# Kernel tuning notes

Hardware: AMD Instinct MI355X
Metric: run time of the kernel (lower is better)

The kernel has to match this reference:

```python
import jax, jax.numpy as jnp
import numpy as np
import math

HID = 512
HEADS = 8
DK = HID // HEADS
B, S, T = 8, 4096, 512


def setup_inputs() -> dict:
    key = jax.random.key(0)
    ks = jax.random.split(key, 12)
    scale = 0.02
    inp = {
        "inputs": jax.random.normal(ks[0], (B, S, HID), dtype=jnp.float32),
        "targets": jax.random.normal(ks[1], (B, T, HID), dtype=jnp.float32),
        "mask": jnp.ones((B, S), dtype=bool),
        "Wq": jax.random.normal(ks[2], (HID, HID), dtype=jnp.float32) * scale,
        "bq": jnp.zeros((HID,), dtype=jnp.float32),
        "Wk": jax.random.normal(ks[3], (HID, HID), dtype=jnp.float32) * scale,
        "bk": jnp.zeros((HID,), dtype=jnp.float32),
        "Wv": jax.random.normal(ks[4], (HID, HID), dtype=jnp.float32) * scale,
        "bv": jnp.zeros((HID,), dtype=jnp.float32),
        "Wo": jax.random.normal(ks[5], (HID, HID), dtype=jnp.float32) * scale,
        "bo": jnp.zeros((HID,), dtype=jnp.float32),
    }
    return inp


def reference(inputs, targets, mask, Wq, bq, Wk, bk, Wv, bv, Wo, bo):
    # PoolingFunction(method='multihead-attention'), dropout=0 (identity),
    # hidden_size == output_size so mapping_function is identity.
    b, t, h = targets.shape
    s = inputs.shape[1]
    Q = (targets @ Wq.T + bq).reshape(b, t, HEADS, DK)
    K = (inputs @ Wk.T + bk).reshape(b, s, HEADS, DK)
    V = (inputs @ Wv.T + bv).reshape(b, s, HEADS, DK)
    # scores: b x heads x tgt x seq (same math as (Q*K).sum(-1)/sqrt(d_k))
    e = jnp.einsum('bthd,bshd->bhts', Q, K) / math.sqrt(DK)
    neg = (1.0 - mask.astype(jnp.float32)) * -1e20  # b x s
    e = e + neg[:, None, None, :]
    a = jax.nn.softmax(e, axis=-1)  # softmax over seq dim
    ctx = jnp.einsum('bhts,bshd->bthd', a, V).reshape(b, t, h)
    return ctx @ Wo.T + bo
```

## Files before the change

kernel.cpp:

```cpp
#include <hip/hip_runtime.h>
#include <hip/hip_bf16.h>
#include <cstdint>
#include <cstddef>

#define HIDN   512
#define NHEADS 8
#define BATCH  8
#define SLEN   4096
#define TLEN   512
#define SSPLIT 4
#define SCHUNK (SLEN / SSPLIT)
#define SCL2   0.18033688f

typedef __attribute__((ext_vector_type(8))) short   bf16x8;
typedef __attribute__((ext_vector_type(4))) float   f32x4;
typedef unsigned short u16;
typedef unsigned int   u32;

__device__ __forceinline__ u32 pkbf(float a, float b) {
    __hip_bfloat162 h = __float22bfloat162_rn(float2{a, b});
    union { __hip_bfloat162 h; u32 u; } un; un.h = h; return un.u;
}
__device__ __forceinline__ u32 pk2(float a, float b) {
    union { float f; u32 u; } ua, ub; ua.f = a; ub.f = b;
    return __builtin_amdgcn_perm(ub.u + 0x8000u, ua.u + 0x8000u, 0x07060302u);
}
__device__ __forceinline__ void gload_lds16(const u16* g, u16* l) {
    __builtin_amdgcn_global_load_lds(
        (const __attribute__((address_space(1))) u32*)g,
        (__attribute__((address_space(3))) u32*)l, 16, 0, 0);
}

__global__ __launch_bounds__(256) void cvt_all(
    const float* __restrict__ X, const float* __restrict__ Tg,
    const float* __restrict__ Wq, const float* __restrict__ Wk,
    const float* __restrict__ Wv, const float* __restrict__ Wo,
    const int* __restrict__ mask,
    u16* __restrict__ Xc, u16* __restrict__ Tc, u16* __restrict__ Wc,
    float* __restrict__ negf)
{
    int i4 = blockIdx.x * 256 + threadIdx.x;
    if (i4 >= 4980736) {
        int off = i4 - 4980736;
        int4 mv = ((const int4*)mask)[off];
        float4 nv;
        nv.x = mv.x ? 0.f : -1e30f; nv.y = mv.y ? 0.f : -1e30f;
        nv.z = mv.z ? 0.f : -1e30f; nv.w = mv.w ? 0.f : -1e30f;
        ((float4*)negf)[off] = nv;
        return;
    }
    const float* s; u16* d; long off;
    if (i4 < 4194304)      { s = X;  d = Xc; off = i4; }
    else if (i4 < 4718592) { s = Tg; d = Tc; off = i4 - 4194304; }
    else {
        int wi = i4 - 4718592; int widx = wi >> 16;
        s = (widx == 0) ? Wq : (widx == 1) ? Wk : (widx == 2) ? Wv : Wo;
        d = Wc + widx * 262144; off = wi & 65535;
    }
    float4 v = *(const float4*)(s + off * 4);
    uint2 o; o.x = pkbf(v.x, v.y); o.y = pkbf(v.z, v.w);
    *(uint2*)(d + off * 4) = o;
}

template<int MODE, int SEQ>
__global__ __launch_bounds__(256)
void gemm_bf16(const u16* __restrict__ A, const u16* __restrict__ Bw,
               const float* __restrict__ bias, void* __restrict__ Yv)
{
    __shared__ u16 As[128 * 32];
    __shared__ u16 Bs[128 * 32];
    const int tid = threadIdx.x;
    const int lane = tid & 63, w = tid >> 6;
    const int m = lane & 15, qd = lane >> 4;
    const int wm = w >> 1, wn = w & 1;
    const int m0 = blockIdx.y * 128, n0 = blockIdx.x * 128;

    f32x4 acc[4][4];
#pragma unroll
    for (int i = 0; i < 4; ++i)
#pragma unroll
        for (int j = 0; j < 4; ++j) acc[i][j] = (f32x4){0.f, 0.f, 0.f, 0.f};

    for (int k0 = 0; k0 < HIDN; k0 += 32) {
#pragma unroll
        for (int r = 0; r < 2; ++r) {
            const int f = tid + r * 256;
            const int row = f >> 2, c8 = (f & 3) * 8;
            const int fb = f & ~63;
            gload_lds16(A  + (size_t)(m0 + row) * HIDN + k0 + c8, As + fb * 8);
            gload_lds16(Bw + (size_t)(n0 + row) * HIDN + k0 + c8, Bs + fb * 8);
        }
        __syncthreads();
        bf16x8 af[4], bf[4];
#pragma unroll
        for (int t = 0; t < 4; ++t) {
            af[t] = *(bf16x8*)&As[(64 * wm + 16 * t + m) * 32 + 8 * qd];
            bf[t] = *(bf16x8*)&Bs[(64 * wn + 16 * t + m) * 32 + 8 * qd];
        }
#pragma unroll
        for (int ti = 0; ti < 4; ++ti)
#pragma unroll
            for (int tj = 0; tj < 4; ++tj)
                acc[ti][tj] = __builtin_amdgcn_mfma_f32_16x16x32_bf16(
                    af[ti], bf[tj], acc[ti][tj], 0, 0, 0);
        __syncthreads();
    }

#pragma unroll
    for (int ti = 0; ti < 4; ++ti) {
        const int gr0 = m0 + 64 * wm + 16 * ti + 4 * qd;
#pragma unroll
        for (int tj = 0; tj < 4; ++tj) {
            const int gcol = n0 + 64 * wn + 16 * tj + m;
            const float bv = bias[gcol];
            if (MODE == 0) {
                float* Y = (float*)Yv;
#pragma unroll
                for (int i = 0; i < 4; ++i)
                    Y[(size_t)(gr0 + i) * HIDN + gcol] = acc[ti][tj][i] + bv;
            } else {
                u16* Y = (u16*)Yv;
                const int b = gr0 / SEQ, h = gcol >> 6, d = gcol & 63;
                const int r = gr0 & (SEQ - 1);
                uint2 o;
                o.x = pkbf(acc[ti][tj][0] + bv, acc[ti][tj][1] + bv);
                o.y = pkbf(acc[ti][tj][2] + bv, acc[ti][tj][3] + bv);
                *(uint2*)&Y[(((size_t)(b * 8 + h)) * 64 + d) * SEQ + r] = o;
            }
        }
    }
}

template<int SEQ>
__global__ __launch_bounds__(256)
void gemm_wxT(const u16* __restrict__ Wm, const u16* __restrict__ X,
              const float* __restrict__ bias, u16* __restrict__ Y)
{
    __shared__ u16 As[128 * 32];
    __shared__ u16 Bs[128 * 32];
    const int tid = threadIdx.x;
    const int lane = tid & 63, w = tid >> 6;
    const int m = lane & 15, qd = lane >> 4;
    const int wm = w >> 1, wn = w & 1;
    const int m0 = blockIdx.y * 128, n0 = blockIdx.x * 128;

    f32x4 acc[4][4];
#pragma unroll
    for (int i = 0; i < 4; ++i)
#pragma unroll
        for (int j = 0; j < 4; ++j) acc[i][j] = (f32x4){0.f, 0.f, 0.f, 0.f};

    for (int k0 = 0; k0 < HIDN; k0 += 32) {
#pragma unroll
        for (int r = 0; r < 2; ++r) {
            const int f = tid + r * 256;
            const int row = f >> 2, c8 = (f & 3) * 8;
            const int fb = f & ~63;
            gload_lds16(Wm + (size_t)(m0 + row) * HIDN + k0 + c8, As + fb * 8);
            gload_lds16(X  + (size_t)(n0 + row) * HIDN + k0 + c8, Bs + fb * 8);
        }
        __syncthreads();
        bf16x8 af[4], bf[4];
#pragma unroll
        for (int t = 0; t < 4; ++t) {
            af[t] = *(bf16x8*)&As[(64 * wm + 16 * t + m) * 32 + 8 * qd];
            bf[t] = *(bf16x8*)&Bs[(64 * wn + 16 * t + m) * 32 + 8 * qd];
        }
#pragma unroll
        for (int ti = 0; ti < 4; ++ti)
#pragma unroll
            for (int tj = 0; tj < 4; ++tj)
                acc[ti][tj] = __builtin_amdgcn_mfma_f32_16x16x32_bf16(
                    af[ti], bf[tj], acc[ti][tj], 0, 0, 0);
        __syncthreads();
    }

#pragma unroll
    for (int ti = 0; ti < 4; ++ti) {
        const int o = m0 + 64 * wm + 16 * ti + 4 * qd;
        const float4 bv = *(const float4*)&bias[o];
        const int h = o >> 6, d0 = o & 63;
#pragma unroll
        for (int tj = 0; tj < 4; ++tj) {
            const int n = n0 + 64 * wn + 16 * tj + m;
            const int b = n / SEQ, r = n & (SEQ - 1);
            uint2 pk;
            pk.x = pkbf(acc[ti][tj][0] + bv.x, acc[ti][tj][1] + bv.y);
            pk.y = pkbf(acc[ti][tj][2] + bv.z, acc[ti][tj][3] + bv.w);
            *(uint2*)&Y[(((size_t)(b * 8 + h)) * SEQ + r) * 64 + d0] = pk;
        }
    }
}

__global__ __launch_bounds__(256, 2)
void attn_part(const u16* __restrict__ Q, const u16* __restrict__ K,
               const u16* __restrict__ Vt, const float* __restrict__ negf,
               float* __restrict__ Opart, float* __restrict__ lpart)
{
    __shared__ char Psh[32768];
    const int tid = threadIdx.x;
    const int lane = tid & 63, w = tid >> 6;
    const int m = lane & 15, qd = lane >> 4;
    const int ti = blockIdx.x, si = blockIdx.y, bh = blockIdx.z;
    const int b = bh >> 3;

    const u16* Qp = Q + ((size_t)bh * TLEN + ti * 256) * 64;
    const u16* Kp = K + (size_t)bh * SLEN * 64;
    const u16* Vp = Vt + (size_t)bh * 64 * SLEN;
    const float* np = negf + (size_t)b * SLEN;

    const int wb = w * 8192 + m * 128;
    int waddr[4], ra0[2], ra1[2];
#pragma unroll
    for (int st = 0; st < 4; ++st) waddr[st] = wb + (((4 * st + qd) ^ m) << 3);
#pragma unroll
    for (int ks = 0; ks < 2; ++ks) {
        const int u0 = 8 * ks + 2 * qd;
        ra0[ks] = wb + (((u0) ^ m) << 3);
        ra1[ks] = wb + (((u0 + 1) ^ m) << 3);
    }

    bf16x8 qf[4][2];
#pragma unroll
    for (int ts = 0; ts < 4; ++ts)
#pragma unroll
        for (int kh = 0; kh < 2; ++kh)
            qf[ts][kh] = *(const bf16x8*)(Qp + (64 * w + 16 * ts + m) * 64 +
                                          32 * kh + 8 * qd);

    f32x4 O[4][4];
#pragma unroll
    for (int ts = 0; ts < 4; ++ts)
#pragma unroll
        for (int dt = 0; dt < 4; ++dt) O[ts][dt] = (f32x4){0.f, 0.f, 0.f, 0.f};
    float lr[4] = {0.f, 0.f, 0.f, 0.f};

    const int s_beg = si * SCHUNK;
    const u16* kp = Kp + (size_t)(s_beg + m) * 64 + 8 * qd;
    const u16* vp0 = Vp + (size_t)m * SLEN + s_beg + 8 * qd;
    const u16* vp1 = vp0 + (size_t)16 * SLEN;
    const u16* vp2 = vp0 + (size_t)32 * SLEN;
    const u16* vp3 = vp0 + (size_t)48 * SLEN;
    const float* npp = np + s_beg + 4 * qd;

#pragma unroll 1
    for (int c = 0; c < SCHUNK; c += 64) {
        bf16x8 kf[4][2];
        kf[0][0] = *(const bf16x8*)(kp + 0);
        kf[0][1] = *(const bf16x8*)(kp + 32);
        kf[1][0] = *(const bf16x8*)(kp + 1024);
        kf[1][1] = *(const bf16x8*)(kp + 1056);
        kf[2][0] = *(const bf16x8*)(kp + 2048);
        kf[2][1] = *(const bf16x8*)(kp + 2080);
        kf[3][0] = *(const bf16x8*)(kp + 3072);
        kf[3][1] = *(const bf16x8*)(kp + 3104);
        float4 ng[4];
        ng[0] = *(const float4*)(npp + 0);
        ng[1] = *(const float4*)(npp + 16);
        ng[2] = *(const float4*)(npp + 32);
        ng[3] = *(const float4*)(npp + 48);
        bf16x8 vf[4][2];
        vf[0][0] = *(const bf16x8*)(vp0 + 0);
        vf[0][1] = *(const bf16x8*)(vp0 + 32);
        vf[1][0] = *(const bf16x8*)(vp1 + 0);
        vf[1][1] = *(const bf16x8*)(vp1 + 32);
        vf[2][0] = *(const bf16x8*)(vp2 + 0);
        vf[2][1] = *(const bf16x8*)(vp2 + 32);
        vf[3][0] = *(const bf16x8*)(vp3 + 0);
        vf[3][1] = *(const bf16x8*)(vp3 + 32);

#pragma unroll
        for (int ts = 0; ts < 4; ++ts) {
            f32x4 S[4];
#pragma unroll
            for (int st = 0; st < 4; ++st) {
                f32x4 cc = (f32x4){0.f, 0.f, 0.f, 0.f};
                cc = __builtin_amdgcn_mfma_f32_16x16x32_bf16(kf[st][0], qf[ts][0], cc, 0, 0, 0);
                cc = __builtin_amdgcn_mfma_f32_16x16x32_bf16(kf[st][1], qf[ts][1], cc, 0, 0, 0);
                S[st] = cc;
            }
            float ls = 0.f;
#pragma unroll
            for (int st = 0; st < 4; ++st) {
                const float p0 = exp2f(fmaf(S[st][0], SCL2, ng[st].x));
                const float p1 = exp2f(fmaf(S[st][1], SCL2, ng[st].y));
                const float p2 = exp2f(fmaf(S[st][2], SCL2, ng[st].z));
                const float p3 = exp2f(fmaf(S[st][3], SCL2, ng[st].w));
                ls += (p0 + p1) + (p2 + p3);
                *(uint2*)&Psh[waddr[st] + ts * 2048] =
                    make_uint2(pk2(p0, p1), pk2(p2, p3));
            }
            lr[ts] += ls;
#pragma unroll
            for (int ks = 0; ks < 2; ++ks) {
                const uint2 r0 = *(uint2*)&Psh[ra0[ks] + ts * 2048];
                const uint2 r1 = *(uint2*)&Psh[ra1[ks] + ts * 2048];
                union { uint4 u; bf16x8 v; } bu;
                bu.u = make_uint4(r0.x, r0.y, r1.x, r1.y);
                O[ts][0] = __builtin_amdgcn_mfma_f32_16x16x32_bf16(vf[0][ks], bu.v, O[ts][0], 0, 0, 0);
                O[ts][1] = __builtin_amdgcn_mfma_f32_16x16x32_bf16(vf[1][ks], bu.v, O[ts][1], 0, 0, 0);
                O[ts][2] = __builtin_amdgcn_mfma_f32_16x16x32_bf16(vf[2][ks], bu.v, O[ts][2], 0, 0, 0);
                O[ts][3] = __builtin_amdgcn_mfma_f32_16x16x32_bf16(vf[3][ks], bu.v, O[ts][3], 0, 0, 0);
            }
        }
        kp += 4096; vp0 += 64; vp1 += 64; vp2 += 64; vp3 += 64; npp += 64;
    }

#pragma unroll
    for (int ts = 0; ts < 4; ++ts) {
        float l = lr[ts];
        l += __shfl_xor(l, 16, 64);
        l += __shfl_xor(l, 32, 64);
        const int t = ti * 256 + 64 * w + 16 * ts + m;
        float* Ob = Opart + (((size_t)(si * 64 + bh)) * 512 + t) * 64;
#pragma unroll
        for (int dt = 0; dt < 4; ++dt)
            *(f32x4*)&Ob[16 * dt + 4 * qd] = O[ts][dt];
        if (qd == 0)
            lpart[((size_t)(si * 64 + bh)) * 512 + t] = l;
    }
}

__global__ __launch_bounds__(256)
void attn_combine(const float* __restrict__ Opart, const float* __restrict__ lpart,
                  u16* __restrict__ ctx)
{
    const int gid = blockIdx.x * 256 + threadIdx.x;
    const int d4 = gid & 15, t = (gid >> 4) & 511, bh = gid >> 13;
    const int b = bh >> 3, h = bh & 7;
    float4 o = {0.f, 0.f, 0.f, 0.f}; float l = 0.f;
#pragma unroll
    for (int si = 0; si < SSPLIT; ++si) {
        const size_t base = ((size_t)(si * 64 + bh)) * 512 + t;
        l += lpart[base];
        const float4 v = *(const float4*)(Opart + base * 64 + d4 * 4);
        o.x += v.x; o.y += v.y; o.z += v.z; o.w += v.w;
    }
    const float r = 1.f / l;
    uint2 pk; pk.x = pkbf(o.x * r, o.y * r); pk.y = pkbf(o.z * r, o.w * r);
    *(uint2*)&ctx[((size_t)(b * 512 + t)) * 512 + h * 64 + d4 * 4] = pk;
}

extern "C" void kernel_launch(void* const* d_in, const int* in_sizes, int n_in,
                              void* d_out, int out_size, void* d_ws, size_t ws_size,
                              hipStream_t stream)
{
    const float* inputs  = (const float*)d_in[0];
    const float* targets = (const float*)d_in[1];
    const int*   mask    = (const int*)d_in[2];
    const float* Wq = (const float*)d_in[3];
    const float* bq = (const float*)d_in[4];
    const float* Wk = (const float*)d_in[5];
    const float* bk = (const float*)d_in[6];
    const float* Wv = (const float*)d_in[7];
    const float* bv = (const float*)d_in[8];
    const float* Wo = (const float*)d_in[9];
    const float* bo = (const float*)d_in[10];

    char* ws = (char*)d_ws;
    u16*   Xc    = (u16*)(ws);
    u16*   Tc    = (u16*)(ws + 33554432);
    u16*   Wc    = (u16*)(ws + 37748736);
    float* negf  = (float*)(ws + 39845888);
    u16*   Qws   = (u16*)(ws + 39976960);
    u16*   Kws   = (u16*)(ws + 44171264);
    u16*   Vtws  = (u16*)(ws + 77725696);
    u16*   Cws   = (u16*)(ws + 111280128);
    float* Opart = (float*)(ws + 115474432);
    float* lpart = (float*)(ws + 149028864);

    cvt_all<<<19488, 256, 0, stream>>>(inputs, targets, Wq, Wk, Wv, Wo, mask,
                                       Xc, Tc, Wc, negf);

    gemm_wxT<TLEN><<<dim3(32, 4),  256, 0, stream>>>(Wc,          Tc, bq, Qws);
    gemm_wxT<SLEN><<<dim3(256, 4), 256, 0, stream>>>(Wc + 262144, Xc, bk, Kws);
    gemm_bf16<2, SLEN><<<dim3(4, 256), 256, 0, stream>>>(Xc, Wc + 524288, bv, Vtws);

    attn_part<<<dim3(2, SSPLIT, 64), 256, 0, stream>>>(Qws, Kws, Vtws, negf,
                                                       Opart, lpart);
    attn_combine<<<2048, 256, 0, stream>>>(Opart, lpart, Cws);

    gemm_bf16<0, TLEN><<<dim3(4, 32), 256, 0, stream>>>(Cws, Wc + 786432, bo,
                                                        (float*)d_out);
}
```

Before: 300.6 us.

## Double-buffer K loads and split QK/PV phases in attention loop

Restructures the attention inner loop so the next K tile and mask values are prefetched into a second register buffer while the current tile's QK scores are computed. All four P tiles are computed first and then consumed in a separate PV phase, with raised wave priority around the PV MFMAs. The manual round-to-nearest bf16 packing is replaced by the hardware v_cvt_pk_bf16_f32 instruction. This raises register pressure from the extra K buffer and hardcodes the trip count (16 tiles per chunk).

```diff
diff --git a/kernel.cpp b/kernel.cpp
--- a/kernel.cpp
+++ b/kernel.cpp
@@ -24,6 +24,11 @@
 __device__ __forceinline__ u32 pk2(float a, float b) {
     union { float f; u32 u; } ua, ub; ua.f = a; ub.f = b;
     return __builtin_amdgcn_perm(ub.u + 0x8000u, ua.u + 0x8000u, 0x07060302u);
+}
+__device__ __forceinline__ u32 cvtpk(float a, float b) {
+    u32 r;
+    asm("v_cvt_pk_bf16_f32 %0, %1, %2" : "=v"(r) : "v"(a), "v"(b));
+    return r;
 }
 __device__ __forceinline__ void gload_lds16(const u16* g, u16* l) {
     __builtin_amdgcn_global_load_lds(
@@ -243,68 +248,108 @@
     const u16* vp3 = vp0 + (size_t)48 * SLEN;
     const float* npp = np + s_beg + 4 * qd;
 
+#define LOADK(kf, ng) do {                                                   \
+        kf[0][0] = *(const bf16x8*)(kp + 0);                                 \
+        kf[0][1] = *(const bf16x8*)(kp + 32);                                \
+        kf[1][0] = *(const bf16x8*)(kp + 1024);                              \
+        kf[1][1] = *(const bf16x8*)(kp + 1056);                              \
+        kf[2][0] = *(const bf16x8*)(kp + 2048);                              \
+        kf[2][1] = *(const bf16x8*)(kp + 2080);                              \
+        kf[3][0] = *(const bf16x8*)(kp + 3072);                              \
+        kf[3][1] = *(const bf16x8*)(kp + 3104);                              \
+        ng[0] = *(const float4*)(npp + 0);                                   \
+        ng[1] = *(const float4*)(npp + 16);                                  \
+        ng[2] = *(const float4*)(npp + 32);                                  \
+        ng[3] = *(const float4*)(npp + 48);                                  \
+        kp += 4096; npp += 64; } while (0)
+
+#define LOADV(vf) do {                                                       \
+        vf[0][0] = *(const bf16x8*)(vp0 + 0);                                \
+        vf[0][1] = *(const bf16x8*)(vp0 + 32);                               \
+        vf[1][0] = *(const bf16x8*)(vp1 + 0);                                \
+        vf[1][1] = *(const bf16x8*)(vp1 + 32);                               \
+        vf[2][0] = *(const bf16x8*)(vp2 + 0);                                \
+        vf[2][1] = *(const bf16x8*)(vp2 + 32);                               \
+        vf[3][0] = *(const bf16x8*)(vp3 + 0);                                \
+        vf[3][1] = *(const bf16x8*)(vp3 + 32);                               \
+        vp0 += 64; vp1 += 64; vp2 += 64; vp3 += 64; } while (0)
+
+#define QKPHASE(kf, ng) do {                                                 \
+        _Pragma("unroll")                                                    \
+        for (int ts = 0; ts < 4; ++ts) {                                     \
+            f32x4 S[4];                                                      \
+            _Pragma("unroll")                                                \
+            for (int st = 0; st < 4; ++st) {                                 \
+                f32x4 cc = (f32x4){0.f, 0.f, 0.f, 0.f};                      \
+                cc = __builtin_amdgcn_mfma_f32_16x16x32_bf16(                \
+                         kf[st][0], qf[ts][0], cc, 0, 0, 0);                 \
+                cc = __builtin_amdgcn_mfma_f32_16x16x32_bf16(                \
+                         kf[st][1], qf[ts][1], cc, 0, 0, 0);                 \
+                S[st] = cc;                                                  \
+            }                                                                \
+            float ls = 0.f;                                                  \
+            _Pragma("unroll")                                                \
+            for (int st = 0; st < 4; ++st) {                                 \
+                const float p0 = exp2f(fmaf(S[st][0], SCL2, ng[st].x));      \
+                const float p1 = exp2f(fmaf(S[st][1], SCL2, ng[st].y));      \
+                const float p2 = exp2f(fmaf(S[st][2], SCL2, ng[st].z));      \
+                const float p3 = exp2f(fmaf(S[st][3], SCL2, ng[st].w));      \
+                ls += (p0 + p1) + (p2 + p3);                                 \
+                *(uint2*)&Psh[waddr[st] + ts * 2048] =                       \
+                    make_uint2(cvtpk(p0, p1), cvtpk(p2, p3));                \
+            }                                                                \
+            lr[ts] += ls;                                                    \
+        } } while (0)
+
+#define PVPHASE(vf) do {                                                     \
+        __builtin_amdgcn_s_setprio(1);                                       \
+        _Pragma("unroll")                                                    \
+        for (int ts = 0; ts < 4; ++ts) {                                     \
+            _Pragma("unroll")                                                \
+            for (int ks = 0; ks < 2; ++ks) {                                 \
+                const uint2 r0 = *(uint2*)&Psh[ra0[ks] + ts * 2048];         \
+                const uint2 r1 = *(uint2*)&Psh[ra1[ks] + ts * 2048];         \
+                union { uint4 u; bf16x8 v; } bu;                             \
+                bu.u = make_uint4(r0.x, r0.y, r1.x, r1.y);                   \
+                O[ts][0] = __builtin_amdgcn_mfma_f32_16x16x32_bf16(          \
+                               vf[0][ks], bu.v, O[ts][0], 0, 0, 0);          \
+                O[ts][1] = __builtin_amdgcn_mfma_f32_16x16x32_bf16(          \
+                               vf[1][ks], bu.v, O[ts][1], 0, 0, 0);          \
+                O[ts][2] = __builtin_amdgcn_mfma_f32_16x16x32_bf16(          \
+                               vf[2][ks], bu.v, O[ts][2], 0, 0, 0);          \
+                O[ts][3] = __builtin_amdgcn_mfma_f32_16x16x32_bf16(          \
+                               vf[3][ks], bu.v, O[ts][3], 0, 0, 0);          \
+            }                                                                \
+        }                                                                    \
+        __builtin_amdgcn_s_setprio(0); } while (0)
+
+    bf16x8 kfA[4][2], kfB[4][2], vf[4][2];
+    float4 ngA[4], ngB[4];
+
+    LOADK(kfA, ngA);
 #pragma unroll 1
-    for (int c = 0; c < SCHUNK; c += 64) {
-        bf16x8 kf[4][2];
-        kf[0][0] = *(const bf16x8*)(kp + 0);
-        kf[0][1] = *(const bf16x8*)(kp + 32);
-        kf[1][0] = *(const bf16x8*)(kp + 1024);
-        kf[1][1] = *(const bf16x8*)(kp + 1056);
-        kf[2][0] = *(const bf16x8*)(kp + 2048);
-        kf[2][1] = *(const bf16x8*)(kp + 2080);
-        kf[3][0] = *(const bf16x8*)(kp + 3072);
-        kf[3][1] = *(const bf16x8*)(kp + 3104);
-        float4 ng[4];
-        ng[0] = *(const float4*)(npp + 0);
-        ng[1] = *(const float4*)(npp + 16);
-        ng[2] = *(const float4*)(npp + 32);
-        ng[3] = *(const float4*)(npp + 48);
-        bf16x8 vf[4][2];
-        vf[0][0] = *(const bf16x8*)(vp0 + 0);
-        vf[0][1] = *(const bf16x8*)(vp0 + 32);
-        vf[1][0] = *(const bf16x8*)(vp1 + 0);
-        vf[1][1] = *(const bf16x8*)(vp1 + 32);
-        vf[2][0] = *(const bf16x8*)(vp2 + 0);
-        vf[2][1] = *(const bf16x8*)(vp2 + 32);
-        vf[3][0] = *(const bf16x8*)(vp3 + 0);
-        vf[3][1] = *(const bf16x8*)(vp3 + 32);
-
-#pragma unroll
-        for (int ts = 0; ts < 4; ++ts) {
-            f32x4 S[4];
-#pragma unroll
-            for (int st = 0; st < 4; ++st) {
-                f32x4 cc = (f32x4){0.f, 0.f, 0.f, 0.f};
-                cc = __builtin_amdgcn_mfma_f32_16x16x32_bf16(kf[st][0], qf[ts][0], cc, 0, 0, 0);
-                cc = __builtin_amdgcn_mfma_f32_16x16x32_bf16(kf[st][1], qf[ts][1], cc, 0, 0, 0);
-                S[st] = cc;
-            }
-            float ls = 0.f;
-#pragma unroll
-            for (int st = 0; st < 4; ++st) {
-                const float p0 = exp2f(fmaf(S[st][0], SCL2, ng[st].x));
-                const float p1 = exp2f(fmaf(S[st][1], SCL2, ng[st].y));
-                const float p2 = exp2f(fmaf(S[st][2], SCL2, ng[st].z));
-                const float p3 = exp2f(fmaf(S[st][3], SCL2, ng[st].w));
-                ls += (p0 + p1) + (p2 + p3);
-                *(uint2*)&Psh[waddr[st] + ts * 2048] =
-                    make_uint2(pk2(p0, p1), pk2(p2, p3));
-            }
-            lr[ts] += ls;
-#pragma unroll
-            for (int ks = 0; ks < 2; ++ks) {
-                const uint2 r0 = *(uint2*)&Psh[ra0[ks] + ts * 2048];
-                const uint2 r1 = *(uint2*)&Psh[ra1[ks] + ts * 2048];
-                union { uint4 u; bf16x8 v; } bu;
-                bu.u = make_uint4(r0.x, r0.y, r1.x, r1.y);
-                O[ts][0] = __builtin_amdgcn_mfma_f32_16x16x32_bf16(vf[0][ks], bu.v, O[ts][0], 0, 0, 0);
-                O[ts][1] = __builtin_amdgcn_mfma_f32_16x16x32_bf16(vf[1][ks], bu.v, O[ts][1], 0, 0, 0);
-                O[ts][2] = __builtin_amdgcn_mfma_f32_16x16x32_bf16(vf[2][ks], bu.v, O[ts][2], 0, 0, 0);
-                O[ts][3] = __builtin_amdgcn_mfma_f32_16x16x32_bf16(vf[3][ks], bu.v, O[ts][3], 0, 0, 0);
-            }
-        }
-        kp += 4096; vp0 += 64; vp1 += 64; vp2 += 64; vp3 += 64; npp += 64;
-    }
+    for (int c = 0; c < 7; ++c) {
+        LOADV(vf);
+        LOADK(kfB, ngB);
+        QKPHASE(kfA, ngA);
+        PVPHASE(vf);
+        LOADV(vf);
+        LOADK(kfA, ngA);
+        QKPHASE(kfB, ngB);
+        PVPHASE(vf);
+    }
+    LOADV(vf);
+    LOADK(kfB, ngB);
+    QKPHASE(kfA, ngA);
+    PVPHASE(vf);
+    LOADV(vf);
+    QKPHASE(kfB, ngB);
+    PVPHASE(vf);
+
+#undef LOADK
+#undef LOADV
+#undef QKPHASE
+#undef PVPHASE
 
 #pragma unroll
     for (int ts = 0; ts < 4; ++ts) {
```

Result: slower. 423.1 us (+40.8%).
